# Optimization experiments

Measured on AMD Instinct MI355X. Metric: run time of the kernel, lower is better.

The kernel has to match this reference:

```python
import jax, jax.numpy as jnp
import numpy as np

# dims
B, S, V, H, D, I, L, SL, P = 1, 2048, 32000, 1024, 512, 4096, 2, 32, 4096
DECAY_FAST, DECAY_SLOW, CONS_RATE, CONS_EVERY = 0.9, 0.99, 0.1, 10


def _ln(x, g, b):
    m = x.mean(-1, keepdims=True)
    v = ((x - m) ** 2).mean(-1, keepdims=True)
    return (x - m) * jax.lax.rsqrt(v + 1e-5) * g + b


def _memory_scan(items, gates, fast0, slow0):
    # items [B,S,D], gates [B,S,SL]; sequential per-timestep memory update
    cons = (jnp.arange(items.shape[1]) % CONS_EVERY) == 0
    def step(carry, x):
        fast, slow = carry
        item, gate, c = x
        fast = DECAY_FAST * fast + gate[:, :, None] * item[:, None, :]
        slow = jnp.where(c, DECAY_SLOW * slow + CONS_RATE * fast, slow)
        fast = jnp.where(c, (1.0 - CONS_RATE) * fast, fast)
        return (fast, slow), None
    (fast, slow), _ = jax.lax.scan(
        step, (fast0, slow0),
        (items.transpose(1, 0, 2), gates.transpose(1, 0, 2), cons))
    return fast, slow


def _forward(input_ids, fast_states, slow_states, emb, pos_emb, W_item, b_item,
             W_q, b_q, rh_W1, rh_b1, rh_W2, rh_b2, gate_W, gate_b, W_out, b_out,
             ln1_g, ln1_b, ffn_W1, ffn_b1, ffn_W2, ffn_b2, ln2_g, ln2_b, fln_g, fln_b):
    b, s = input_ids.shape
    h = emb[input_ids] + pos_emb[:s][None]  # [B,S,H]
    new_fast, new_slow = [], []
    for l in range(W_item.shape[0]):
        items = h @ W_item[l] + b_item[l]          # [B,S,D]
        query = h @ W_q[l] + b_q[l]                # [B,S,H]
        # retrieval head -> unit-norm unbinding keys
        k1 = jax.nn.gelu(items @ rh_W1[l] + rh_b1[l])
        keys = k1 @ rh_W2[l] + rh_b2[l]
        keys = keys / (jnp.linalg.norm(keys, axis=-1, keepdims=True) + 1e-6)
        fast0, slow0 = fast_states[l], slow_states[l]  # [B,SL,D]
        # retrieval uses the initial (constant-within-sequence) states, so it
        # vectorizes over seq: slot attention + hadamard unbinding
        mem = jnp.concatenate([fast0, slow0], axis=1)  # [B,2*SL,D]
        scores = jnp.einsum('bsd,bnd->bsn', keys, mem) / jnp.sqrt(jnp.float32(D))
        attn = jax.nn.softmax(scores, axis=-1)
        retrieved = jnp.einsum('bsn,bnd->bsd', attn, mem) * keys  # [B,S,D]
        gates = jax.nn.sigmoid(jnp.concatenate([h, retrieved], -1) @ gate_W[l] + gate_b[l])
        fast_gates = gates[..., :SL]
        fast, slow = _memory_scan(items, fast_gates, fast0, slow0)
        new_fast.append(fast)
        new_slow.append(slow)
        out = jnp.concatenate([query, retrieved], -1) @ W_out[l] + b_out[l]
        h = _ln(h + out, ln1_g[l], ln1_b[l])
        ffn = jax.nn.gelu(h @ ffn_W1[l] + ffn_b1[l]) @ ffn_W2[l] + ffn_b2[l]
        h = _ln(h + ffn, ln2_g[l], ln2_b[l])
    h = _ln(h, fln_g, fln_b)
    logits = jnp.einsum('bsh,vh->bsv', h, emb)  # tied lm_head
    return logits, jnp.stack(new_fast), jnp.stack(new_slow)


def setup_inputs() -> dict:
    key = jax.random.key(0)
    def rn(i, shape, scale=0.02):
        return jax.random.normal(jax.random.fold_in(key, i), shape, dtype=jnp.float32) * scale
    z = lambda shape: jnp.zeros(shape, jnp.float32)
    return dict(
        input_ids=jax.random.randint(jax.random.fold_in(key, 0), (B, S), 0, V),
        fast_states=rn(100, (L, B, SL, D), 0.5),
        slow_states=rn(101, (L, B, SL, D), 0.5),
        emb=rn(1, (V, H)),
        pos_emb=rn(2, (P, H)),
        W_item=rn(3, (L, H, D)), b_item=z((L, D)),
        W_q=rn(4, (L, H, H)), b_q=z((L, H)),
        rh_W1=rn(5, (L, D, 2 * D)), rh_b1=z((L, 2 * D)),
        rh_W2=rn(6, (L, 2 * D, D)), rh_b2=z((L, D)),
        gate_W=rn(7, (L, H + D, 2 * SL)), gate_b=z((L, 2 * SL)),
        W_out=rn(8, (L, H + D, H)), b_out=z((L, H)),
        ln1_g=jnp.ones((L, H)), ln1_b=z((L, H)),
        ffn_W1=rn(9, (L, H, I)), ffn_b1=z((L, I)),
        ffn_W2=rn(10, (L, I, H)), ffn_b2=z((L, H)),
        ln2_g=jnp.ones((L, H)), ln2_b=z((L, H)),
        fln_g=jnp.ones((H,)), fln_b=z((H,)),
    )


def reference(input_ids, fast_states, slow_states, emb, pos_emb, W_item, b_item,
              W_q, b_q, rh_W1, rh_b1, rh_W2, rh_b2, gate_W, gate_b, W_out, b_out,
              ln1_g, ln1_b, ffn_W1, ffn_b1, ffn_W2, ffn_b2, ln2_g, ln2_b, fln_g, fln_b):
    return _forward(input_ids, fast_states, slow_states, emb, pos_emb, W_item, b_item,
                    W_q, b_q, rh_W1, rh_b1, rh_W2, rh_b2, gate_W, gate_b, W_out, b_out,
                    ln1_g, ln1_b, ffn_W1, ffn_b1, ffn_W2, ffn_b2, ln2_g, ln2_b, fln_g, fln_b)
```

## Files before the change

### kernel.cpp

```cpp
#include <hip/hip_runtime.h>
#include <hip/hip_bf16.h>
#include <stdint.h>

typedef __hip_bfloat16 bf16;
typedef float f32x4 __attribute__((ext_vector_type(4)));
typedef short s16x8 __attribute__((ext_vector_type(8)));
typedef short s16x4 __attribute__((ext_vector_type(4)));

#define DEV __device__ __forceinline__

static constexpr int S_ = 2048, H_ = 1024, D_ = 512, I_ = 4096, V_ = 32000;
static constexpr int SLn = 32, Lc = 2;
static constexpr size_t LOGITS_N = (size_t)S_ * V_;

DEV float gelu_f(float x) {
    float x3 = x * x * x;
    return 0.5f * x * (1.f + tanhf(0.7978845608028654f * (x + 0.044715f * x3)));
}

#define AS1(p) ((const __attribute__((address_space(1))) void*)(uintptr_t)(p))
#define AS3(p) ((__attribute__((address_space(3))) void*)(uint32_t)(uintptr_t)(p))

template <int BM, int BN, int TH, int WM, int WN, int FLAGS>
__global__ __launch_bounds__(TH, (TH == 512) ? 2 : 3) void gemm_p5(
    const bf16* __restrict__ A, int lda, const bf16* __restrict__ BT,
    const float* __restrict__ bias, float* __restrict__ Cf, int ldf,
    bf16* __restrict__ Cb, int ldb2, int K, int Mt, int Nt) {
    constexpr int FM = BM / (WM * 16), FN = BN / (WN * 16);
    constexpr int CA = (BM * 4) / TH, CB = (BN * 4) / TH, CH = CA + CB;
    constexpr int NPH = (FM * FN >= 32) ? 2 : 1;
    constexpr int FMP = FM / NPH;
    constexpr int BUFS = (BM + BN) * 32;
    __shared__ short lds[4 * BUFS];
    const int tid = threadIdx.x, lane = tid & 63;
    const int wm = (tid >> 6) / WN, wn = (tid >> 6) % WN;

    int nwg = Mt * Nt;
    int bid = blockIdx.x, wgid = bid;
    if ((nwg & 7) == 0) {
        int cpx = nwg >> 3;
        wgid = (bid & 7) * cpx + (bid >> 3);
    }
    const int m0 = (wgid % Mt) * BM, n0 = (wgid / Mt) * BN;

    const bf16* aS[CA];
    const bf16* bS[CB];
#pragma unroll
    for (int c = 0; c < CA; ++c) {
        int L = (c * TH + tid) * 16;
        int sidx = L >> 10, w = L & 1023;
        int r16 = w >> 6;
        int c2 = (w & 63) ^ (((r16 >> 3) & 1) << 5);
        aS[c] = A + (size_t)(m0 + sidx * 16 + r16) * lda + (c2 >> 1);
    }
#pragma unroll
    for (int c = 0; c < CB; ++c) {
        int L = (c * TH + tid) * 16;
        int sidx = L >> 10, w = L & 1023;
        int r16 = w >> 6;
        int c2 = (w & 63) ^ (((r16 >> 3) & 1) << 5);
        bS[c] = BT + (size_t)(n0 + sidx * 16 + r16) * K + (c2 >> 1);
    }

    auto stageA = [&](int kt) {
        short* dst = &lds[(kt & 3) * BUFS];
#pragma unroll
        for (int c = 0; c < CA; ++c)
            __builtin_amdgcn_global_load_lds(AS1(aS[c] + kt * 32), AS3(dst + (c * TH + tid) * 8), 16, 0, 0);
    };
    auto stageB = [&](int kt) {
        short* dst = &lds[(kt & 3) * BUFS + BM * 32];
#pragma unroll
        for (int c = 0; c < CB; ++c)
            __builtin_amdgcn_global_load_lds(AS1(bS[c] + kt * 32), AS3(dst + (c * TH + tid) * 8), 16, 0, 0);
    };

    const int laneoff = ((lane & 15) * 64 + ((((lane >> 4) * 8) ^ (((lane >> 3) & 1) << 4)) << 1)) >> 1;

    f32x4 acc[FM][FN];
#pragma unroll
    for (int i = 0; i < FM; i++)
#pragma unroll
        for (int j = 0; j < FN; j++)
#pragma unroll
            for (int r = 0; r < 4; r++) acc[i][j][r] = 0.f;

    const int NT = K >> 5;
    stageA(0); stageB(0);
    stageA(1); stageB(1);
    stageA(2); stageB(2);
    asm volatile("s_waitcnt vmcnt(%0)" ::"n"(2 * CH) : "memory");
    __builtin_amdgcn_s_barrier();

    for (int t = 0; t < NT; ++t) {
        const short* as = &lds[(t & 3) * BUFS];
        const short* bs = as + BM * 32;
        s16x8 bf[FN];
#pragma unroll
        for (int p = 0; p < NPH; ++p) {
            s16x8 af[FMP];
#pragma unroll
            for (int i = 0; i < FMP; i++)
                af[i] = *(const s16x8*)&as[(wm * FM + p * FMP + i) * 512 + laneoff];
            if (p == 0) {
#pragma unroll
                for (int j = 0; j < FN; j++)
                    bf[j] = *(const s16x8*)&bs[(wn * FN + j) * 512 + laneoff];
            }
            if (t + 3 < NT) {
                if (NPH == 1) {
                    stageA(t + 3);
                    stageB(t + 3);
                } else if (p == 0) {
                    stageA(t + 3);
                } else {
                    stageB(t + 3);
                }
            }
            if (p == NPH - 1 && t + 1 < NT) {
                const int ahead = NT - 2 - t;
                if (ahead >= 2)
                    asm volatile("s_waitcnt vmcnt(%0)" ::"n"(2 * CH) : "memory");
                else if (ahead == 1)
                    asm volatile("s_waitcnt vmcnt(%0)" ::"n"(CH) : "memory");
                else
                    asm volatile("s_waitcnt vmcnt(0)" ::: "memory");
            }
            __builtin_amdgcn_s_barrier();
            __builtin_amdgcn_sched_barrier(0);
            __builtin_amdgcn_s_setprio(1);
#pragma unroll
            for (int i = 0; i < FMP; i++)
#pragma unroll
                for (int j = 0; j < FN; j++)
                    acc[p * FMP + i][j] =
                        __builtin_amdgcn_mfma_f32_16x16x32_bf16(af[i], bf[j], acc[p * FMP + i][j], 0, 0, 0);
            __builtin_amdgcn_s_setprio(0);
            __builtin_amdgcn_s_barrier();
        }
    }

#pragma unroll
    for (int i = 0; i < FM; i++) {
        int gr0 = m0 + (wm * FM + i) * 16 + ((lane >> 4) << 2);
#pragma unroll
        for (int j = 0; j < FN; j++) {
            int gc = n0 + (wn * FN + j) * 16 + (lane & 15);
            float bv = (FLAGS & 1) ? bias[gc] : 0.f;
#pragma unroll
            for (int r = 0; r < 4; r++) {
                float v = acc[i][j][r] + bv;
                if (FLAGS & 2) v = gelu_f(v);
                if (FLAGS & 4) Cf[(size_t)(gr0 + r) * ldf + gc] = v;
                if (FLAGS & 8) Cb[(size_t)(gr0 + r) * ldb2 + gc] = __float2bfloat16(v);
            }
        }
    }
}

__global__ __launch_bounds__(256) void transpose_bf16_kernel(const float* __restrict__ W,
                                                             bf16* __restrict__ WT, int K, int N) {
    __shared__ float t[32][33];
    int tx = threadIdx.x & 31, ty = threadIdx.x >> 5;
    int kb = blockIdx.y * 32, nb = blockIdx.x * 32;
#pragma unroll
    for (int i = 0; i < 4; i++)
        t[ty + 8 * i][tx] = W[(size_t)(kb + ty + 8 * i) * N + nb + tx];
    __syncthreads();
#pragma unroll
    for (int i = 0; i < 4; i++)
        WT[(size_t)(nb + ty + 8 * i) * K + kb + tx] = __float2bfloat16(t[tx][ty + 8 * i]);
}

__global__ void conv_bf16_kernel(const float* __restrict__ src, bf16* __restrict__ dst) {
    size_t i = (size_t)blockIdx.x * 256 + threadIdx.x;
    f32x4 v = ((const f32x4*)src)[i];
    s16x4 o;
#pragma unroll
    for (int j = 0; j < 4; j++) {
        bf16 h = __float2bfloat16(v[j]);
        o[j] = *(short*)&h;
    }
    ((s16x4*)dst)[i] = o;
}

__global__ void embed_kernel(const int* __restrict__ ids, const float* __restrict__ emb,
                             const float* __restrict__ pos, float* __restrict__ hF,
                             bf16* __restrict__ hB) {
    int t = blockIdx.x, tid = threadIdx.x;
    int id = ids[t];
    f32x4 v = ((const f32x4*)(emb + (size_t)id * H_))[tid];
    f32x4 q = ((const f32x4*)(pos + (size_t)t * H_))[tid];
    v = v + q;
    ((f32x4*)(hF + (size_t)t * H_))[tid] = v;
    s16x4 o;
#pragma unroll
    for (int j = 0; j < 4; j++) {
        bf16 h = __float2bfloat16(v[j]);
        o[j] = *(short*)&h;
    }
    ((s16x4*)(hB + (size_t)t * 1536))[tid] = o;
}

__global__ __launch_bounds__(256) void ln_kernel(const float* __restrict__ x,
                                                 const float* __restrict__ res,
                                                 const float* __restrict__ g,
                                                 const float* __restrict__ b,
                                                 float* __restrict__ of, bf16* __restrict__ ob,
                                                 int ldo) {
    __shared__ float red[8];
    int row = blockIdx.x, tid = threadIdx.x, lane = tid & 63, wid = tid >> 6;
    const float* xr = x + (size_t)row * H_;
    float v[4];
#pragma unroll
    for (int j = 0; j < 4; j++) {
        int c = tid + 256 * j;
        v[j] = xr[c] + (res ? res[(size_t)row * H_ + c] : 0.f);
    }
    float s = v[0] + v[1] + v[2] + v[3];
#pragma unroll
    for (int o = 32; o; o >>= 1) s += __shfl_xor(s, o);
    if (!lane) red[wid] = s;
    __syncthreads();
    float mean = (red[0] + red[1] + red[2] + red[3]) * (1.f / H_);
    float q = 0.f;
#pragma unroll
    for (int j = 0; j < 4; j++) {
        float d = v[j] - mean;
        q += d * d;
    }
#pragma unroll
    for (int o = 32; o; o >>= 1) q += __shfl_xor(q, o);
    if (!lane) red[4 + wid] = q;
    __syncthreads();
    float var = (red[4] + red[5] + red[6] + red[7]) * (1.f / H_);
    float rstd = rsqrtf(var + 1e-5f);
#pragma unroll
    for (int j = 0; j < 4; j++) {
        int c = tid + 256 * j;
        float o2 = (v[j] - mean) * rstd * g[c] + b[c];
        if (of) of[(size_t)row * H_ + c] = o2;
        if (ob) ob[(size_t)row * ldo + c] = __float2bfloat16(o2);
    }
}

__global__ void memt_kernel(const float* __restrict__ fast0, const float* __restrict__ slow0,
                            float* __restrict__ memT) {
    int idx = blockIdx.x * 256 + threadIdx.x;
    int d = idx >> 6, n = idx & 63;
    const float* m = (n < 32) ? fast0 + (size_t)n * D_ : slow0 + (size_t)(n - 32) * D_;
    memT[idx] = m[d];
}

__global__ __launch_bounds__(256) void attn_kernel(const float* __restrict__ keys,
                                                   const float* __restrict__ memT,
                                                   const float* __restrict__ fast0,
                                                   const float* __restrict__ slow0,
                                                   bf16* __restrict__ qr, bf16* __restrict__ hr) {
    __shared__ float klds[4][512];
    int wid = threadIdx.x >> 6, lane = threadIdx.x & 63;
    int r = blockIdx.x * 4 + wid;
    float kv[8], ss = 0.f;
#pragma unroll
    for (int j = 0; j < 8; j++) {
        kv[j] = keys[(size_t)r * D_ + lane + 64 * j];
        ss += kv[j] * kv[j];
    }
#pragma unroll
    for (int o = 32; o; o >>= 1) ss += __shfl_xor(ss, o);
    float inv = 1.f / (sqrtf(ss) + 1e-6f);
#pragma unroll
    for (int j = 0; j < 8; j++) {
        kv[j] *= inv;
        klds[wid][lane + 64 * j] = kv[j];
    }
    __syncthreads();
    float s0 = 0.f, s1 = 0.f, s2 = 0.f, s3 = 0.f;
#pragma unroll 8
    for (int d = 0; d < 512; d += 4) {
        s0 = fmaf(klds[wid][d + 0], memT[(d + 0) * 64 + lane], s0);
        s1 = fmaf(klds[wid][d + 1], memT[(d + 1) * 64 + lane], s1);
        s2 = fmaf(klds[wid][d + 2], memT[(d + 2) * 64 + lane], s2);
        s3 = fmaf(klds[wid][d + 3], memT[(d + 3) * 64 + lane], s3);
    }
    float s = (s0 + s1 + s2 + s3) * 0.044194173824159216f;
    float m = s;
#pragma unroll
    for (int o = 32; o; o >>= 1) m = fmaxf(m, __shfl_xor(m, o));
    float p = expf(s - m);
    float sum = p;
#pragma unroll
    for (int o = 32; o; o >>= 1) sum += __shfl_xor(sum, o);
    float pn = p / sum;
    float rv[8];
#pragma unroll
    for (int j = 0; j < 8; j++) rv[j] = 0.f;
    for (int n2 = 0; n2 < 64; ++n2) {
        float a2 = __shfl(pn, n2);
        const float* m2 = (n2 < 32) ? (fast0 + (size_t)n2 * D_) : (slow0 + (size_t)(n2 - 32) * D_);
#pragma unroll
        for (int j = 0; j < 8; j++) rv[j] = fmaf(a2, m2[lane + 64 * j], rv[j]);
    }
#pragma unroll
    for (int j = 0; j < 8; j++) {
        bf16 o = __float2bfloat16(rv[j] * kv[j]);
        qr[(size_t)r * 1536 + 1024 + lane + 64 * j] = o;
        hr[(size_t)r * 1536 + 1024 + lane + 64 * j] = o;
    }
}

__global__ void coef_kernel(float* __restrict__ coef) {
    int t = blockIdx.x * 256 + threadIdx.x;
    int j0 = (t + 9) / 10;
    float a = powf(0.9f, (float)(2047 - t + 205 - j0));
    float b = 0.f;
    for (int j = j0; j < 205; ++j)
        b += powf(0.9f, (float)(10 * j - t + j - j0)) * powf(0.99f, (float)(204 - j));
    b *= 0.1f;
    coef[t] = a;
    coef[2048 + t] = b;
    if (t == 0) {
        coef[4096] = powf(0.99f, 205.f);
        float cfs = 0.f;
        for (int j = 0; j < 205; ++j)
            cfs += powf(0.9f, (float)(11 * j + 1)) * powf(0.99f, (float)(204 - j));
        coef[4097] = 0.1f * cfs;
    }
}

__global__ void sigcoef_kernel(const float* __restrict__ raw, const float* __restrict__ coef,
                               float* __restrict__ ga, float* __restrict__ gb) {
    int i = blockIdx.x * 256 + threadIdx.x;
    int r = i >> 5, n = i & 31;
    float g = 1.f / (1.f + expf(-raw[r * 64 + n]));
    ga[i] = g * coef[r];
    gb[i] = g * coef[2048 + r];
}

__global__ __launch_bounds__(256) void scan_part_kernel(const float* __restrict__ items,
                                                        const float* __restrict__ ga,
                                                        const float* __restrict__ gb,
                                                        float* __restrict__ pF,
                                                        float* __restrict__ pS) {
    int tid = threadIdx.x;
    int d = (blockIdx.x & 7) * 64 + (tid & 63);
    int mg = (blockIdx.x >> 3) & 1;
    int tc = blockIdx.x >> 4;
    int m0 = mg * 16 + (tid >> 6) * 4;
    float aF[4] = {0.f, 0.f, 0.f, 0.f}, aS[4] = {0.f, 0.f, 0.f, 0.f};
    for (int t = tc * 128; t < tc * 128 + 128; ++t) {
        float it = items[(size_t)t * D_ + d];
#pragma unroll
        for (int j = 0; j < 4; j++) {
            aF[j] = fmaf(ga[t * 32 + m0 + j], it, aF[j]);
            aS[j] = fmaf(gb[t * 32 + m0 + j], it, aS[j]);
        }
    }
#pragma unroll
    for (int j = 0; j < 4; j++) {
        pF[((size_t)tc * 32 + m0 + j) * D_ + d] = aF[j];
        pS[((size_t)tc * 32 + m0 + j) * D_ + d] = aS[j];
    }
}

__global__ __launch_bounds__(256) void scan_reduce_kernel(const float* __restrict__ pF,
                                                          const float* __restrict__ pS,
                                                          const float* __restrict__ coef,
                                                          const float* __restrict__ fast0,
                                                          const float* __restrict__ slow0,
                                                          float* __restrict__ fastO,
                                                          float* __restrict__ slowO) {
    int i = blockIdx.x * 256 + threadIdx.x;
    float f = 0.f, s = 0.f;
#pragma unroll
    for (int c = 0; c < 16; c++) {
        f += pF[(size_t)c * 32 * D_ + i];
        s += pS[(size_t)c * 32 * D_ + i];
    }
    fastO[i] = f;
    slowO[i] = s + coef[4096] * slow0[i] + coef[4097] * fast0[i];
}

static inline void gemmM(hipStream_t st, const bf16* A, int lda, const bf16* BT,
                         const float* bias, float* Cf, int ldf, bf16* Cb, int ldb2,
                         int M, int N, int K, int flags) {
    int Mt = M / 128, Nt = N / 64;
    dim3 g(Mt * Nt), b(256);
#define GCASE(fl)                                                                             \
    if (flags == fl) {                                                                        \
        gemm_p5<128, 64, 256, 2, 2, fl><<<g, b, 0, st>>>(A, lda, BT, bias, Cf, ldf, Cb, ldb2, \
                                                         K, Mt, Nt);                          \
        return;                                                                               \
    }
    GCASE(13)
    GCASE(9)
    GCASE(11)
    GCASE(5)
#undef GCASE
}

static inline void transp(hipStream_t st, const float* W, bf16* WT, int K, int N) {
    transpose_bf16_kernel<<<dim3(N / 32, K / 32), 256, 0, st>>>(W, WT, K, N);
}

extern "C" void kernel_launch(void* const* d_in, const int* in_sizes, int n_in,
                              void* d_out, int out_size, void* d_ws, size_t ws_size,
                              hipStream_t stream) {
    const int* ids = (const int*)d_in[0];
    const float* fastS = (const float*)d_in[1];
    const float* slowS = (const float*)d_in[2];
    const float* emb = (const float*)d_in[3];
    const float* pos = (const float*)d_in[4];
    const float* W_item = (const float*)d_in[5];
    const float* b_item = (const float*)d_in[6];
    const float* W_q = (const float*)d_in[7];
    const float* b_q = (const float*)d_in[8];
    const float* rh_W1 = (const float*)d_in[9];
    const float* rh_b1 = (const float*)d_in[10];
    const float* rh_W2 = (const float*)d_in[11];
    const float* rh_b2 = (const float*)d_in[12];
    const float* gate_W = (const float*)d_in[13];
    const float* gate_b = (const float*)d_in[14];
    const float* W_out = (const float*)d_in[15];
    const float* b_out = (const float*)d_in[16];
    const float* ln1_g = (const float*)d_in[17];
    const float* ln1_b = (const float*)d_in[18];
    const float* ffn_W1 = (const float*)d_in[19];
    const float* ffn_b1 = (const float*)d_in[20];
    const float* ffn_W2 = (const float*)d_in[21];
    const float* ffn_b2 = (const float*)d_in[22];
    const float* ln2_g = (const float*)d_in[23];
    const float* ln2_b = (const float*)d_in[24];
    const float* fln_g = (const float*)d_in[25];
    const float* fln_b = (const float*)d_in[26];
    float* outP = (float*)d_out;

    size_t off = 0;
    char* base = (char*)d_ws;
    auto alloc = [&](size_t n) -> char* {
        char* p = base + off;
        off += (n + 255) & ~(size_t)255;
        return p;
    };
    bf16* wItemT = (bf16*)alloc((size_t)Lc * D_ * H_ * 2);
    bf16* wQT = (bf16*)alloc((size_t)Lc * H_ * H_ * 2);
    bf16* rh1T = (bf16*)alloc((size_t)Lc * (2 * D_) * D_ * 2);
    bf16* rh2T = (bf16*)alloc((size_t)Lc * D_ * (2 * D_) * 2);
    bf16* wOutT = (bf16*)alloc((size_t)Lc * H_ * 1536 * 2);
    bf16* f1T = (bf16*)alloc((size_t)Lc * I_ * H_ * 2);
    bf16* f2T = (bf16*)alloc((size_t)Lc * H_ * I_ * 2);
    bf16* gWT = (bf16*)alloc((size_t)Lc * 64 * 1536 * 2);
    bf16* embB = (bf16*)alloc((size_t)V_ * H_ * 2);
    float* hF = (float*)alloc((size_t)S_ * H_ * 4);
    bf16* hrB = (bf16*)alloc((size_t)S_ * 1536 * 2);
    bf16* hB = hrB;
    float* itemsF = (float*)alloc((size_t)S_ * D_ * 4);
    bf16* itemsB = (bf16*)alloc((size_t)S_ * D_ * 2);
    bf16* qrB = (bf16*)alloc((size_t)S_ * 1536 * 2);
    bf16* k1B = (bf16*)alloc((size_t)S_ * (2 * D_) * 2);
    float* keysF = (float*)alloc((size_t)S_ * D_ * 4);
    float* outF = (float*)alloc((size_t)S_ * H_ * 4);
    bf16* ffn1B = (bf16*)alloc((size_t)S_ * I_ * 2);
    float* gRawF = (float*)alloc((size_t)S_ * 64 * 4);
    float* gaF = (float*)alloc((size_t)S_ * SLn * 4);
    float* gbF = (float*)alloc((size_t)S_ * SLn * 4);
    float* coefF = (float*)alloc(4200 * 4);
    float* memT = (float*)alloc((size_t)D_ * 64 * 4);
    float* pF = (float*)alloc((size_t)16 * SLn * D_ * 4);
    float* pS = (float*)alloc((size_t)16 * SLn * D_ * 4);

    coef_kernel<<<8, 256, 0, stream>>>(coefF);
    for (int l = 0; l < Lc; ++l) {
        transp(stream, W_item + (size_t)l * H_ * D_, wItemT + (size_t)l * D_ * H_, H_, D_);
        transp(stream, W_q + (size_t)l * H_ * H_, wQT + (size_t)l * H_ * H_, H_, H_);
        transp(stream, rh_W1 + (size_t)l * D_ * 2 * D_, rh1T + (size_t)l * 2 * D_ * D_, D_, 2 * D_);
        transp(stream, rh_W2 + (size_t)l * 2 * D_ * D_, rh2T + (size_t)l * D_ * 2 * D_, 2 * D_, D_);
        transp(stream, W_out + (size_t)l * 1536 * H_, wOutT + (size_t)l * H_ * 1536, 1536, H_);
        transp(stream, ffn_W1 + (size_t)l * H_ * I_, f1T + (size_t)l * I_ * H_, H_, I_);
        transp(stream, ffn_W2 + (size_t)l * I_ * H_, f2T + (size_t)l * H_ * I_, I_, H_);
        transp(stream, gate_W + (size_t)l * 1536 * 64, gWT + (size_t)l * 64 * 1536, 1536, 64);
    }
    conv_bf16_kernel<<<(int)((size_t)V_ * H_ / 4 / 256), 256, 0, stream>>>(emb, embB);
    embed_kernel<<<S_, 256, 0, stream>>>(ids, emb, pos, hF, hB);

    for (int l = 0; l < Lc; ++l) {
        const float* fast0 = fastS + (size_t)l * SLn * D_;
        const float* slow0 = slowS + (size_t)l * SLn * D_;
        gemmM(stream, hB, 1536, wItemT + (size_t)l * D_ * H_, b_item + l * D_, itemsF, D_,
              itemsB, D_, S_, D_, H_, 13);
        gemmM(stream, hB, 1536, wQT + (size_t)l * H_ * H_, b_q + l * H_, nullptr, 0, qrB, 1536,
              S_, H_, H_, 9);
        gemmM(stream, itemsB, D_, rh1T + (size_t)l * 2 * D_ * D_, rh_b1 + l * 2 * D_, nullptr, 0,
              k1B, 2 * D_, S_, 2 * D_, D_, 11);
        gemmM(stream, k1B, 2 * D_, rh2T + (size_t)l * D_ * 2 * D_, rh_b2 + l * D_, keysF, D_,
              nullptr, 0, S_, D_, 2 * D_, 5);
        memt_kernel<<<128, 256, 0, stream>>>(fast0, slow0, memT);
        attn_kernel<<<S_ / 4, 256, 0, stream>>>(keysF, memT, fast0, slow0, qrB, hrB);
        gemmM(stream, hrB, 1536, gWT + (size_t)l * 64 * 1536, gate_b + l * 64, gRawF, 64,
              nullptr, 0, S_, 64, 1536, 5);
        sigcoef_kernel<<<S_ * SLn / 256, 256, 0, stream>>>(gRawF, coefF, gaF, gbF);
        scan_part_kernel<<<256, 256, 0, stream>>>(itemsF, gaF, gbF, pF, pS);
        scan_reduce_kernel<<<64, 256, 0, stream>>>(
            pF, pS, coefF, fast0, slow0, outP + LOGITS_N + (size_t)l * SLn * D_,
            outP + LOGITS_N + (size_t)Lc * SLn * D_ + (size_t)l * SLn * D_);
        gemmM(stream, qrB, 1536, wOutT + (size_t)l * H_ * 1536, b_out + l * H_, outF, H_,
              nullptr, 0, S_, H_, 1536, 5);
        ln_kernel<<<S_, 256, 0, stream>>>(hF, outF, ln1_g + l * H_, ln1_b + l * H_, hF, hB, 1536);
        gemmM(stream, hB, 1536, f1T + (size_t)l * I_ * H_, ffn_b1 + l * I_, nullptr, 0, ffn1B,
              I_, S_, I_, H_, 11);
        gemmM(stream, ffn1B, I_, f2T + (size_t)l * H_ * I_, ffn_b2 + l * H_, outF, H_, nullptr,
              0, S_, H_, I_, 5);
        ln_kernel<<<S_, 256, 0, stream>>>(hF, outF, ln2_g + l * H_, ln2_b + l * H_, hF, hB, 1536);
    }
    ln_kernel<<<S_, 256, 0, stream>>>(hF, nullptr, fln_g, fln_b, nullptr, hB, 1536);
    gemm_p5<256, 256, 512, 2, 4, 4><<<1000, 512, 0, stream>>>(hB, 1536, embB, nullptr, outP, V_,
                                                              nullptr, 0, H_, 8, 125);
}
```

Measured before the change: 923.8 us.

## Shrink GEMM pipeline to three LDS stages and retile the vocab projection

The GEMM's shared-memory ring goes from four buffers with a prefetch distance of three down to three buffers with a prefetch distance of two, using explicit slot counters. Launch bounds now take a template minimum-waves value, set to 4 for the 128x64 GEMMs and 2 for the logits GEMM. The final vocab projection changes from 256x256 tiles with 512 threads to 256x128 tiles with 256 threads and twice as many workgroups. The smaller LDS footprint is meant to allow higher occupancy, at the cost of less latency hiding per workgroup and more register pressure.

```diff
diff --git a/kernel.cpp b/kernel.cpp
--- a/kernel.cpp
+++ b/kernel.cpp
@@ -21,8 +21,8 @@
 #define AS1(p) ((const __attribute__((address_space(1))) void*)(uintptr_t)(p))
 #define AS3(p) ((__attribute__((address_space(3))) void*)(uint32_t)(uintptr_t)(p))
 
-template <int BM, int BN, int TH, int WM, int WN, int FLAGS>
-__global__ __launch_bounds__(TH, (TH == 512) ? 2 : 3) void gemm_p5(
+template <int BM, int BN, int TH, int WM, int WN, int MINW, int FLAGS>
+__global__ __launch_bounds__(TH, MINW) void gemm_p6(
     const bf16* __restrict__ A, int lda, const bf16* __restrict__ BT,
     const float* __restrict__ bias, float* __restrict__ Cf, int ldf,
     bf16* __restrict__ Cb, int ldb2, int K, int Mt, int Nt) {
@@ -30,8 +30,8 @@
     constexpr int CA = (BM * 4) / TH, CB = (BN * 4) / TH, CH = CA + CB;
     constexpr int NPH = (FM * FN >= 32) ? 2 : 1;
     constexpr int FMP = FM / NPH;
-    constexpr int BUFS = (BM + BN) * 32;
-    __shared__ short lds[4 * BUFS];
+    constexpr int SLOT = (BM + BN) * 32;
+    __shared__ short lds[3 * SLOT];
     const int tid = threadIdx.x, lane = tid & 63;
     const int wm = (tid >> 6) / WN, wn = (tid >> 6) % WN;
 
@@ -62,14 +62,14 @@
         bS[c] = BT + (size_t)(n0 + sidx * 16 + r16) * K + (c2 >> 1);
     }
 
-    auto stageA = [&](int kt) {
-        short* dst = &lds[(kt & 3) * BUFS];
+    auto stageA = [&](int kt, int slot) {
+        short* dst = &lds[slot * SLOT];
 #pragma unroll
         for (int c = 0; c < CA; ++c)
             __builtin_amdgcn_global_load_lds(AS1(aS[c] + kt * 32), AS3(dst + (c * TH + tid) * 8), 16, 0, 0);
     };
-    auto stageB = [&](int kt) {
-        short* dst = &lds[(kt & 3) * BUFS + BM * 32];
+    auto stageB = [&](int kt, int slot) {
+        short* dst = &lds[slot * SLOT + BM * 32];
 #pragma unroll
         for (int c = 0; c < CB; ++c)
             __builtin_amdgcn_global_load_lds(AS1(bS[c] + kt * 32), AS3(dst + (c * TH + tid) * 8), 16, 0, 0);
@@ -86,14 +86,14 @@
             for (int r = 0; r < 4; r++) acc[i][j][r] = 0.f;
 
     const int NT = K >> 5;
-    stageA(0); stageB(0);
-    stageA(1); stageB(1);
-    stageA(2); stageB(2);
-    asm volatile("s_waitcnt vmcnt(%0)" ::"n"(2 * CH) : "memory");
+    stageA(0, 0); stageB(0, 0);
+    stageA(1, 1); stageB(1, 1);
+    asm volatile("s_waitcnt vmcnt(%0)" ::"n"(CH) : "memory");
     __builtin_amdgcn_s_barrier();
 
+    int sl = 0, ss = 2;
     for (int t = 0; t < NT; ++t) {
-        const short* as = &lds[(t & 3) * BUFS];
+        const short* as = &lds[sl * SLOT];
         const short* bs = as + BM * 32;
         s16x8 bf[FN];
 #pragma unroll
@@ -107,23 +107,20 @@
                 for (int j = 0; j < FN; j++)
                     bf[j] = *(const s16x8*)&bs[(wn * FN + j) * 512 + laneoff];
             }
-            if (t + 3 < NT) {
+            if (t + 2 < NT) {
                 if (NPH == 1) {
-                    stageA(t + 3);
-                    stageB(t + 3);
+                    stageA(t + 2, ss);
+                    stageB(t + 2, ss);
                 } else if (p == 0) {
-                    stageA(t + 3);
+                    stageA(t + 2, ss);
                 } else {
-                    stageB(t + 3);
+                    stageB(t + 2, ss);
                 }
             }
-            if (p == NPH - 1 && t + 1 < NT) {
-                const int ahead = NT - 2 - t;
-                if (ahead >= 2)
-                    asm volatile("s_waitcnt vmcnt(%0)" ::"n"(2 * CH) : "memory");
-                else if (ahead == 1)
+            if (p == NPH - 1) {
+                if (t + 2 < NT)
                     asm volatile("s_waitcnt vmcnt(%0)" ::"n"(CH) : "memory");
-                else
+                else if (t + 1 < NT)
                     asm volatile("s_waitcnt vmcnt(0)" ::: "memory");
             }
             __builtin_amdgcn_s_barrier();
@@ -138,6 +135,8 @@
             __builtin_amdgcn_s_setprio(0);
             __builtin_amdgcn_s_barrier();
         }
+        sl = (sl == 2) ? 0 : sl + 1;
+        ss = (ss == 2) ? 0 : ss + 1;
     }
 
 #pragma unroll
@@ -386,11 +385,11 @@
                          int M, int N, int K, int flags) {
     int Mt = M / 128, Nt = N / 64;
     dim3 g(Mt * Nt), b(256);
-#define GCASE(fl)                                                                             \
-    if (flags == fl) {                                                                        \
-        gemm_p5<128, 64, 256, 2, 2, fl><<<g, b, 0, st>>>(A, lda, BT, bias, Cf, ldf, Cb, ldb2, \
-                                                         K, Mt, Nt);                          \
-        return;                                                                               \
+#define GCASE(fl)                                                                              \
+    if (flags == fl) {                                                                         \
+        gemm_p6<128, 64, 256, 2, 2, 4, fl><<<g, b, 0, st>>>(A, lda, BT, bias, Cf, ldf, Cb,     \
+                                                            ldb2, K, Mt, Nt);                  \
+        return;                                                                                \
     }
     GCASE(13)
     GCASE(9)
@@ -513,6 +512,6 @@
         ln_kernel<<<S_, 256, 0, stream>>>(hF, outF, ln2_g + l * H_, ln2_b + l * H_, hF, hB, 1536);
     }
     ln_kernel<<<S_, 256, 0, stream>>>(hF, nullptr, fln_g, fln_b, nullptr, hB, 1536);
-    gemm_p5<256, 256, 512, 2, 4, 4><<<1000, 512, 0, stream>>>(hB, 1536, embB, nullptr, outP, V_,
-                                                              nullptr, 0, H_, 8, 125);
-}
+    gemm_p6<256, 128, 256, 2, 2, 2, 4><<<2000, 256, 0, stream>>>(hB, 1536, embB, nullptr, outP,
+                                                                 V_, nullptr, 0, H_, 8, 250);
+}
```

New measurement: 1.003 ms. 8.5% more time.
